# Performance work log

Hardware: AMD Instinct MI355X
Metric: run time of the kernel (lower is better)

## Reference

```python
import jax, jax.numpy as jnp
import numpy as np

N, E = 50000, 800000
D_IN, HID, HEADS, D_OUT = 128, 32, 4, 40
NEG_SLOPE = 0.2
BN_EPS = 1e-5


def gat_conv(x, src, dst, W, a_src, a_dst, b, heads, ch):
    """PyG-style GATConv (eval mode, self-loops already appended to src/dst)."""
    n = x.shape[0]
    h = (x @ W).reshape(n, heads, ch)                      # [N,H,C]
    al_src = jnp.einsum('nhc,hc->nh', h, a_src)            # [N,H]
    al_dst = jnp.einsum('nhc,hc->nh', h, a_dst)
    e = jax.nn.leaky_relu(al_src[src] + al_dst[dst], NEG_SLOPE)  # [Etot,H]
    # segment softmax over incoming edges of each dst node
    e_max = jax.ops.segment_max(e, dst, num_segments=n)
    e = jnp.exp(e - e_max[dst])
    denom = jax.ops.segment_sum(e, dst, num_segments=n)
    alpha = e / (denom[dst] + 1e-16)                        # [Etot,H]
    msg = h[src] * alpha[:, :, None]                        # [Etot,H,C]
    out = jax.ops.segment_sum(msg, dst, num_segments=n)     # [N,H,C]
    return out.reshape(n, heads * ch) + b


def bn_eval(x, g, b, m, v):
    return (x - m) * jax.lax.rsqrt(v + BN_EPS) * g + b


def setup_inputs() -> dict:
    key = jax.random.key(0)
    ks = jax.random.split(key, 24)
    p = lambda k, s: jax.random.normal(k, s, jnp.float32) * 0.1
    inp = {
        'x': jax.random.normal(ks[0], (N, D_IN), jnp.float32),
        'edge_index': jax.random.randint(ks[1], (2, E), 0, N),
        'W1': p(ks[2], (D_IN, HEADS * HID)),
        'a_src1': p(ks[3], (HEADS, HID)), 'a_dst1': p(ks[4], (HEADS, HID)),
        'b1': jnp.zeros((HEADS * HID,), jnp.float32),
        'W2': p(ks[5], (HEADS * HID, HEADS * HID)),
        'a_src2': p(ks[6], (HEADS, HID)), 'a_dst2': p(ks[7], (HEADS, HID)),
        'b2': jnp.zeros((HEADS * HID,), jnp.float32),
        'W3': p(ks[8], (HEADS * HID, D_OUT)),
        'a_src3': p(ks[9], (1, D_OUT)), 'a_dst3': p(ks[10], (1, D_OUT)),
        'b3': jnp.zeros((D_OUT,), jnp.float32),
        'bn1_g': jnp.ones((HEADS * HID,), jnp.float32),
        'bn1_b': jnp.zeros((HEADS * HID,), jnp.float32),
        'bn1_m': p(ks[11], (HEADS * HID,)),
        'bn1_v': jax.random.uniform(ks[12], (HEADS * HID,), jnp.float32) + 0.5,
        'bn2_g': jnp.ones((HEADS * HID,), jnp.float32),
        'bn2_b': jnp.zeros((HEADS * HID,), jnp.float32),
        'bn2_m': p(ks[13], (HEADS * HID,)),
        'bn2_v': jax.random.uniform(ks[14], (HEADS * HID,), jnp.float32) + 0.5,
    }
    return inp


def reference(x, edge_index, W1, a_src1, a_dst1, b1, W2, a_src2, a_dst2, b2,
              W3, a_src3, a_dst3, b3, bn1_g, bn1_b, bn1_m, bn1_v,
              bn2_g, bn2_b, bn2_m, bn2_v):
    n = x.shape[0]
    loop = jnp.arange(n, dtype=edge_index.dtype)
    src = jnp.concatenate([edge_index[0], loop])   # add self loops (PyG default)
    dst = jnp.concatenate([edge_index[1], loop])

    h = gat_conv(x, src, dst, W1, a_src1, a_dst1, b1, HEADS, HID)
    h = jax.nn.relu(h)
    h = bn_eval(h, bn1_g, bn1_b, bn1_m, bn1_v)      # dropout = identity (eval)

    h = gat_conv(h, src, dst, W2, a_src2, a_dst2, b2, HEADS, HID)
    h = jax.nn.relu(h)
    h = bn_eval(h, bn2_g, bn2_b, bn2_m, bn2_v)

    h = gat_conv(h, src, dst, W3, a_src3, a_dst3, b3, 1, D_OUT)
    return jax.nn.log_softmax(h, axis=1)
```

## Files before the change

### kernel.cpp

```cpp
#include <hip/hip_runtime.h>
#include <hip/hip_bf16.h>
#include <math.h>

using bf16 = __hip_bfloat16;
using frag8 = __attribute__((ext_vector_type(8))) short;
using f32x4 = __attribute__((ext_vector_type(4))) float;

#define LEAKY 0.2f
#define BN_EPS 1e-5f
#define NEGBIG -1e30f
#define BSHIFT 9

__device__ __forceinline__ float lrelu(float z){ return fmaxf(z, LEAKY * z); }
__device__ __forceinline__ float bflo(unsigned u){ return __uint_as_float(u << 16); }
__device__ __forceinline__ float bfhi(unsigned u){ return __uint_as_float(u & 0xffff0000u); }
__device__ __forceinline__ unsigned pk(float a, float b){
  unsigned ua = __float_as_uint(a), ub = __float_as_uint(b);
  ua += 0x7fffu + ((ua >> 16) & 1u);
  ub += 0x7fffu + ((ub >> 16) & 1u);
  return (ua >> 16) | (ub & 0xffff0000u);
}
__device__ __forceinline__ float ldf(const void* p, size_t i, int isbf){
  if (isbf) return (float)((const bf16*)p)[i];
  return ((const float*)p)[i];
}

union U4F8 { uint4 u; frag8 f; };

__device__ __forceinline__ frag8 load_a_pairs(const unsigned* __restrict__ X2, int node, int k0){
  U4F8 v; v.u = *((const uint4*)(X2 + (size_t)node*64 + (k0 >> 1))); return v.f;
}
__device__ __forceinline__ frag8 load_a_f32(const float* __restrict__ X, int node, int k0){
  float4 q0 = *((const float4*)(X + (size_t)node*128 + k0));
  float4 q1 = *((const float4*)(X + (size_t)node*128 + k0 + 4));
  U4F8 v; v.u = make_uint4(pk(q0.x,q0.y), pk(q0.z,q0.w), pk(q1.x,q1.y), pk(q1.z,q1.w));
  return v.f;
}

__global__ void init_detect(int* bcnt, const unsigned short* __restrict__ w1bits,
                            int* flag){
  __shared__ int cntr;
  if (threadIdx.x == 0) cntr = 0;
  bcnt[threadIdx.x] = 0;
  __syncthreads();
  unsigned u = w1bits[threadIdx.x * 2];
  int e = (u >> 7) & 0xff;
  atomicAdd(&cntr, (e >= 64 && e <= 140) ? 1 : 0);
  __syncthreads();
  if (threadIdx.x == 0) *flag = (cntr >= 160) ? 1 : 0;
}

__global__ __launch_bounds__(256) void wtrans(
    const void* __restrict__ W1, const void* __restrict__ W2,
    const void* __restrict__ W3, const int* __restrict__ flagp,
    unsigned short* __restrict__ WT1, unsigned short* __restrict__ WT2,
    unsigned short* __restrict__ WT3){
  const int isbf = *flagp;
  const int g = blockIdx.x*256 + threadIdx.x;
  if (g < 16384){
    int k = g >> 7, nn = g & 127;
    unsigned short v1, v2;
    if (isbf){
      v1 = ((const unsigned short*)W1)[g];
      v2 = ((const unsigned short*)W2)[g];
    } else {
      v1 = (unsigned short)(pk(((const float*)W1)[g], 0.f) & 0xffffu);
      v2 = (unsigned short)(pk(((const float*)W2)[g], 0.f) & 0xffffu);
    }
    WT1[nn*128 + k] = v1;
    WT2[nn*128 + k] = v2;
  }
  if (g < 8192){
    int c = g & 63, k = g >> 6;
    if (c < 48){
      unsigned short v = 0;
      if (c < 40){
        if (isbf) v = ((const unsigned short*)W3)[k*40 + c];
        else      v = (unsigned short)(pk(((const float*)W3)[k*40 + c], 0.f) & 0xffffu);
      }
      WT3[c*128 + k] = v;
    }
  }
}

__global__ __launch_bounds__(256) void hist(const int* __restrict__ dst,
                                            int* bcnt, int e, int n){
  __shared__ int lb[256];
  const int t = threadIdx.x;
  lb[t] = 0;
  __syncthreads();
  const int c0 = blockIdx.x*4096;
  const int lim = min(4096, e - c0);
  for (int i = t; i < lim; i += 256){
    int d = dst[c0 + i];
    if ((unsigned)d < (unsigned)n)
      atomicAdd(&lb[min(d >> BSHIFT, 255)], 1);
  }
  __syncthreads();
  if (lb[t]) atomicAdd(&bcnt[t], lb[t]);
}

__global__ void bscan(const int* __restrict__ bcnt, int* bstart, int* bpos){
  __shared__ int s[256];
  int t = threadIdx.x;
  int v = bcnt[t];
  s[t] = v;
  __syncthreads();
  for (int off = 1; off < 256; off <<= 1){
    int x = (t >= off) ? s[t-off] : 0;
    __syncthreads();
    s[t] += x;
    __syncthreads();
  }
  int st = s[t] - v;
  bstart[t] = st;
  bpos[t] = st;
}

__global__ __launch_bounds__(256) void bsort(const int* __restrict__ src,
                                             const int* __restrict__ dst,
                                             int* bpos, int2* __restrict__ ebuf,
                                             int e, int n){
  __shared__ int lh[256], lo[256], gb[256];
  __shared__ int tot_s;
  __shared__ int2 buf[4096];
  const int t = threadIdx.x;
  const int c0 = blockIdx.x*4096;
  if (c0 >= e) return;
  const int lim = min(4096, e - c0);
  lh[t] = 0;
  __syncthreads();
  int2 ev[16]; int bk[16];
  #pragma unroll
  for (int j = 0; j < 16; ++j){
    const int i = j*256 + t;
    const bool valid = i < lim;
    int s = 0, d = 0;
    if (valid){ s = src[c0 + i]; d = dst[c0 + i]; }
    ev[j] = make_int2(s, d);
    bk[j] = (valid && (unsigned)d < (unsigned)n) ? min(d >> BSHIFT, 255) : -1;
    if (bk[j] >= 0) atomicAdd(&lh[bk[j]], 1);
  }
  __syncthreads();
  const int v = lh[t];
  lo[t] = v;
  __syncthreads();
  for (int off = 1; off < 256; off <<= 1){
    int x = (t >= off) ? lo[t-off] : 0;
    __syncthreads();
    lo[t] += x;
    __syncthreads();
  }
  if (t == 255) tot_s = lo[255];
  lo[t] -= v;
  if (v) gb[t] = atomicAdd(&bpos[t], v);
  lh[t] = 0;
  __syncthreads();
  #pragma unroll
  for (int j = 0; j < 16; ++j){
    if (bk[j] >= 0){
      int r = atomicAdd(&lh[bk[j]], 1);
      buf[lo[bk[j]] + r] = ev[j];
    }
  }
  __syncthreads();
  const int tot = tot_s;
  for (int i = t; i < tot; i += 256){
    int2 sd = buf[i];
    int b = min(sd.y >> BSHIFT, 255);
    ebuf[gb[b] + (i - lo[b])] = sd;
  }
}

__global__ __launch_bounds__(256) void bfinal(const int2* __restrict__ ebuf,
    const int* __restrict__ bstart, const int* __restrict__ bpos,
    int* __restrict__ cnt, int* __restrict__ start, int* __restrict__ col, int n){
  __shared__ int deg[512], off[512], ps[256];
  const int b = blockIdx.x, t = threadIdx.x;
  const int n0 = b << BSHIFT;
  const int e0 = bstart[b], e1 = bpos[b];
  deg[t] = 0; deg[t + 256] = 0;
  __syncthreads();
  for (int i = e0 + t; i < e1; i += 256)
    atomicAdd(&deg[ebuf[i].y - n0], 1);
  __syncthreads();
  int p = deg[2*t] + deg[2*t + 1];
  ps[t] = p;
  __syncthreads();
  for (int o = 1; o < 256; o <<= 1){
    int x = (t >= o) ? ps[t - o] : 0;
    __syncthreads();
    ps[t] += x;
    __syncthreads();
  }
  int ex = ps[t] - p;
  off[2*t]     = ex;
  off[2*t + 1] = ex + deg[2*t];
  __syncthreads();
  #pragma unroll
  for (int j = t; j < 512; j += 256){
    int node = n0 + j;
    if (node < n){ cnt[node] = deg[j]; start[node] = e0 + off[j]; }
  }
  __syncthreads();
  for (int i = e0 + t; i < e1; i += 256){
    int2 sd = ebuf[i];
    int r = atomicAdd(&off[sd.y - n0], 1);
    col[e0 + r] = sd.x;
  }
}

__global__ __launch_bounds__(256) void gemm_al_mfma(
    const void* __restrict__ X, int xkind,
    const unsigned short* __restrict__ WT,
    const void* __restrict__ Wsrc, const void* __restrict__ Wdst,
    const int* __restrict__ flagp,
    unsigned* __restrict__ H2, float* __restrict__ AL, float* __restrict__ AD,
    int n, int ntiles)
{
  const int isbf = *flagp;
  const int t = threadIdx.x;
  const int w = t >> 6;
  const int lane = t & 63;
  const int m = lane & 15, quad = lane >> 4;

  frag8 bf[4][2];
  #pragma unroll
  for (int s = 0; s < 4; ++s)
    #pragma unroll
    for (int ct = 0; ct < 2; ++ct){
      int colc = w*32 + ct*16 + m;
      int k0 = s*32 + quad*8;
      U4F8 v; v.u = *((const uint4*)(WT + colc*128 + k0));
      bf[s][ct] = v.f;
    }
  float avv[2], dvv[2];
  #pragma unroll
  for (int ct = 0; ct < 2; ++ct){
    int colc = w*32 + ct*16 + m;
    avv[ct] = ldf(Wsrc, colc, isbf);
    dvv[ct] = ldf(Wdst, colc, isbf);
  }
  const bool pairs = (xkind == 1) || isbf;

  for (int tile = blockIdx.x; tile < ntiles; tile += gridDim.x){
    const int mb = tile*16;
    int nodeA = mb + m; if (nodeA >= n) nodeA = n - 1;
    frag8 af[4];
    #pragma unroll
    for (int s = 0; s < 4; ++s){
      int k0 = s*32 + quad*8;
      af[s] = pairs ? load_a_pairs((const unsigned*)X, nodeA, k0)
                    : load_a_f32((const float*)X, nodeA, k0);
    }
    f32x4 acc0 = {0.f,0.f,0.f,0.f}, acc1 = {0.f,0.f,0.f,0.f};
    #pragma unroll
    for (int s = 0; s < 4; ++s){
      acc0 = __builtin_amdgcn_mfma_f32_16x16x32_bf16(af[s], bf[s][0], acc0, 0,0,0);
      acc1 = __builtin_amdgcn_mfma_f32_16x16x32_bf16(af[s], bf[s][1], acc1, 0,0,0);
    }
    #pragma unroll
    for (int r = 0; r < 4; ++r){
      int g = mb + quad*4 + r;
      float v0 = acc0[r], v1 = acc1[r];
      unsigned u0 = pk(v0, __shfl_xor(v0, 1));
      unsigned u1 = pk(v1, __shfl_xor(v1, 1));
      bool ok = g < n;
      if (((lane & 1) == 0) && ok){
        H2[(size_t)g*64 + w*16 + (m >> 1)]     = u0;
        H2[(size_t)g*64 + w*16 + 8 + (m >> 1)] = u1;
      }
      float s1 = v0*avv[0] + v1*avv[1];
      float s2 = v0*dvv[0] + v1*dvv[1];
      s1 += __shfl_xor(s1,1); s1 += __shfl_xor(s1,2); s1 += __shfl_xor(s1,4); s1 += __shfl_xor(s1,8);
      s2 += __shfl_xor(s2,1); s2 += __shfl_xor(s2,2); s2 += __shfl_xor(s2,4); s2 += __shfl_xor(s2,8);
      if (m == 0 && ok){ AL[g*4 + w] = s1; AD[g*4 + w] = s2; }
    }
  }
}

__global__ __launch_bounds__(256) void gemm3_mfma(
    const unsigned* __restrict__ X2, const unsigned short* __restrict__ WT,
    const void* __restrict__ Wsrc, const void* __restrict__ Wdst,
    const int* __restrict__ flagp,
    unsigned* __restrict__ H3, float* __restrict__ AL, float* __restrict__ AD,
    int n, int ntiles)
{
  const int isbf = *flagp;
  const int t = threadIdx.x;
  const int w = t >> 6;
  const int lane = t & 63;
  const int m = lane & 15, quad = lane >> 4;

  frag8 bf[4][3];
  float avv[3], dvv[3];
  #pragma unroll
  for (int ct = 0; ct < 3; ++ct){
    int colc = ct*16 + m;
    #pragma unroll
    for (int s = 0; s < 4; ++s){
      int k0 = s*32 + quad*8;
      U4F8 v; v.u = *((const uint4*)(WT + colc*128 + k0));
      bf[s][ct] = v.f;
    }
    avv[ct] = (colc < 40) ? ldf(Wsrc, colc, isbf) : 0.f;
    dvv[ct] = (colc < 40) ? ldf(Wdst, colc, isbf) : 0.f;
  }

  for (int tg = blockIdx.x; tg*4 < ntiles; tg += gridDim.x){
    const int tile = tg*4 + w;
    if (tile >= ntiles) continue;
    const int mb = tile*16;
    int nodeA = mb + m; if (nodeA >= n) nodeA = n - 1;
    frag8 af[4];
    #pragma unroll
    for (int s = 0; s < 4; ++s)
      af[s] = load_a_pairs(X2, nodeA, s*32 + quad*8);
    f32x4 acc[3];
    #pragma unroll
    for (int ct = 0; ct < 3; ++ct) acc[ct] = (f32x4){0.f,0.f,0.f,0.f};
    #pragma unroll
    for (int s = 0; s < 4; ++s){
      acc[0] = __builtin_amdgcn_mfma_f32_16x16x32_bf16(af[s], bf[s][0], acc[0], 0,0,0);
      acc[1] = __builtin_amdgcn_mfma_f32_16x16x32_bf16(af[s], bf[s][1], acc[1], 0,0,0);
      acc[2] = __builtin_amdgcn_mfma_f32_16x16x32_bf16(af[s], bf[s][2], acc[2], 0,0,0);
    }
    #pragma unroll
    for (int r = 0; r < 4; ++r){
      int g = mb + quad*4 + r;
      bool ok = g < n;
      float ps = 0.f, pd = 0.f;
      #pragma unroll
      for (int ct = 0; ct < 3; ++ct){
        float v = acc[ct][r];
        ps += v*avv[ct]; pd += v*dvv[ct];
        unsigned u = pk(v, __shfl_xor(v, 1));
        bool stok = ((lane & 1) == 0) && ok && (ct < 2 || m < 8);
        if (stok) H3[(size_t)g*20 + ct*8 + (m >> 1)] = u;
      }
      ps += __shfl_xor(ps,1); ps += __shfl_xor(ps,2); ps += __shfl_xor(ps,4); ps += __shfl_xor(ps,8);
      pd += __shfl_xor(pd,1); pd += __shfl_xor(pd,2); pd += __shfl_xor(pd,4); pd += __shfl_xor(pd,8);
      if (m == 0 && ok){ AL[g] = ps; AD[g] = pd; }
    }
  }
}

__global__ __launch_bounds__(256) void agg4(
    const unsigned* __restrict__ H2,
    const float* __restrict__ ALf, const float* __restrict__ ADf,
    const int* __restrict__ cnt, const int* __restrict__ start, const int* __restrict__ col,
    const void* __restrict__ bias, const void* __restrict__ bng, const void* __restrict__ bnb,
    const void* __restrict__ bnm,  const void* __restrict__ bnv,
    const int* __restrict__ flagp,
    unsigned* __restrict__ Hout, int n)
{
  const int isbf = *flagp;
  const int wave = threadIdx.x >> 6;
  const int lane = threadIdx.x & 63;
  const int node = blockIdx.x*4 + wave;
  if (node >= n) return;
  const int head = lane >> 4;
  const float ad = ADf[node*4 + head];
  const int eu = (lane >> 2) & 7;
  const int eh = lane & 3;
  const float ade = ADf[node*4 + eh];
  const int base = start[node], deg = cnt[node];

  float accL, accH, l;
  {
    float e = __expf(lrelu(ALf[node*4 + head] + ad));
    unsigned h = H2[(size_t)node*64 + lane];
    l = e; accL = e * bflo(h); accH = e * bfhi(h);
  }

  const int nb8 = deg >> 3, rem = deg & 7;
  int sva[8], svb[8];
  if (nb8){
    #pragma unroll
    for (int u = 0; u < 8; ++u) sva[u] = col[base + u];
  } else if (rem){
    const int lim = rem - 1;
    #pragma unroll
    for (int u = 0; u < 8; ++u) sva[u] = col[base + (u < lim ? u : lim)];
  }
  for (int b = 0; b < nb8; ++b){
    unsigned hv[8];
    #pragma unroll
    for (int u = 0; u < 8; ++u) hv[u] = H2[(size_t)sva[u]*64 + lane];
    float ave = ALf[sva[eu]*4 + eh];
    if (b + 1 < nb8){
      const int nbb = base + (b + 1)*8;
      #pragma unroll
      for (int u = 0; u < 8; ++u) svb[u] = col[nbb + u];
    } else if (rem){
      const int tb = base + nb8*8, lim = rem - 1;
      #pragma unroll
      for (int u = 0; u < 8; ++u) svb[u] = col[tb + (u < lim ? u : lim)];
    }
    float ew = __expf(lrelu(ave + ade));
    #pragma unroll
    for (int u = 0; u < 8; ++u){
      float e = __shfl(ew, (u << 2) + head);
      l += e;
      accL = fmaf(e, bflo(hv[u]), accL);
      accH = fmaf(e, bfhi(hv[u]), accH);
    }
    #pragma unroll
    for (int u = 0; u < 8; ++u) sva[u] = svb[u];
  }
  if (rem){
    unsigned hv[8];
    #pragma unroll
    for (int u = 0; u < 8; ++u) hv[u] = H2[(size_t)sva[u]*64 + lane];
    float ave = ALf[sva[eu]*4 + eh];
    float ew = __expf(lrelu(ave + ade));
    #pragma unroll
    for (int u = 0; u < 8; ++u){
      float e = (u < rem) ? __shfl(ew, (u << 2) + head) : 0.f;
      l += e;
      accL = fmaf(e, bflo(hv[u]), accL);
      accH = fmaf(e, bfhi(hv[u]), accH);
    }
  }

  const float rl = 1.f / l;
  const int c0 = 2*lane, c1 = c0 + 1;
  float v0 = fmaxf(accL*rl + ldf(bias,c0,isbf), 0.f);
  v0 = (v0 - ldf(bnm,c0,isbf)) * rsqrtf(ldf(bnv,c0,isbf) + BN_EPS) * ldf(bng,c0,isbf) + ldf(bnb,c0,isbf);
  float v1 = fmaxf(accH*rl + ldf(bias,c1,isbf), 0.f);
  v1 = (v1 - ldf(bnm,c1,isbf)) * rsqrtf(ldf(bnv,c1,isbf) + BN_EPS) * ldf(bng,c1,isbf) + ldf(bnb,c1,isbf);
  Hout[(size_t)node*64 + lane] = pk(v0, v1);
}

__global__ __launch_bounds__(256) void agg1(
    const unsigned* __restrict__ H3,
    const float* __restrict__ AL, const float* __restrict__ AD,
    const int* __restrict__ cnt, const int* __restrict__ start, const int* __restrict__ col,
    const void* __restrict__ b3, const int* __restrict__ flagp,
    void* __restrict__ out, int n)
{
  const int isbf = *flagp;
  const int t = threadIdx.x;
  const int p = t & 31;
  const int node = blockIdx.x*8 + (t >> 5);
  if (node >= n) return;
  const float ad = AD[node];
  const bool act = p < 20;
  const int eu = p & 7;
  const int base = start[node], deg = cnt[node];

  float accL, accH, l;
  {
    float e = __expf(lrelu(AL[node] + ad));
    unsigned h = act ? H3[(size_t)node*20 + p] : 0u;
    l = e; accL = e * bflo(h); accH = e * bfhi(h);
  }

  const int nb8 = deg >> 3, rem = deg & 7;
  int sva[8], svb[8];
  if (nb8){
    #pragma unroll
    for (int u = 0; u < 8; ++u) sva[u] = col[base + u];
  } else if (rem){
    const int lim = rem - 1;
    #pragma unroll
    for (int u = 0; u < 8; ++u) sva[u] = col[base + (u < lim ? u : lim)];
  }
  for (int b = 0; b < nb8; ++b){
    unsigned hv[8];
    #pragma unroll
    for (int u = 0; u < 8; ++u) hv[u] = act ? H3[(size_t)sva[u]*20 + p] : 0u;
    float ave = AL[sva[eu]];
    if (b + 1 < nb8){
      const int nbb = base + (b + 1)*8;
      #pragma unroll
      for (int u = 0; u < 8; ++u) svb[u] = col[nbb + u];
    } else if (rem){
      const int tb = base + nb8*8, lim = rem - 1;
      #pragma unroll
      for (int u = 0; u < 8; ++u) svb[u] = col[tb + (u < lim ? u : lim)];
    }
    float ew = __expf(lrelu(ave + ad));
    #pragma unroll
    for (int u = 0; u < 8; ++u){
      float e = __shfl(ew, u, 32);
      l += e;
      accL = fmaf(e, bflo(hv[u]), accL);
      accH = fmaf(e, bfhi(hv[u]), accH);
    }
    #pragma unroll
    for (int u = 0; u < 8; ++u) sva[u] = svb[u];
  }
  if (rem){
    unsigned hv[8];
    #pragma unroll
    for (int u = 0; u < 8; ++u) hv[u] = act ? H3[(size_t)sva[u]*20 + p] : 0u;
    float ave = AL[sva[eu]];
    float ew = __expf(lrelu(ave + ad));
    #pragma unroll
    for (int u = 0; u < 8; ++u){
      float e = (u < rem) ? __shfl(ew, u, 32) : 0.f;
      l += e;
      accL = fmaf(e, bflo(hv[u]), accL);
      accH = fmaf(e, bfhi(hv[u]), accH);
    }
  }

  const float rl = 1.f / l;
  const int c0 = 2*p;
  float z0 = act ? (accL*rl + ldf(b3, c0,     isbf)) : NEGBIG;
  float z1 = act ? (accH*rl + ldf(b3, c0 + 1, isbf)) : NEGBIG;
  float mx = fmaxf(z0, z1);
  #pragma unroll
  for (int off = 1; off < 32; off <<= 1) mx = fmaxf(mx, __shfl_xor(mx, off));
  float pp = act ? (__expf(z0 - mx) + __expf(z1 - mx)) : 0.f;
  float sum = pp;
  #pragma unroll
  for (int off = 1; off < 32; off <<= 1) sum += __shfl_xor(sum, off);
  if (act){
    float lg = __logf(sum);
    float r0 = z0 - mx - lg, r1 = z1 - mx - lg;
    if (isbf) ((unsigned*)out)[(size_t)node*20 + p] = pk(r0, r1);
    else      ((float2*)out)[(size_t)node*20 + p] = make_float2(r0, r1);
  }
}

extern "C" void kernel_launch(void* const* d_in, const int* in_sizes, int n_in,
                              void* d_out, int out_size, void* d_ws, size_t ws_size,
                              hipStream_t stream)
{
  (void)n_in; (void)out_size; (void)ws_size;
  const void* x    = d_in[0];
  const int*  ei   = (const int*)d_in[1];
  const void* W1   = d_in[2];
  const void* as1  = d_in[3];
  const void* ad1  = d_in[4];
  const void* b1   = d_in[5];
  const void* W2   = d_in[6];
  const void* as2  = d_in[7];
  const void* ad2  = d_in[8];
  const void* b2   = d_in[9];
  const void* W3   = d_in[10];
  const void* as3  = d_in[11];
  const void* ad3  = d_in[12];
  const void* b3   = d_in[13];
  const void* bn1g = d_in[14];
  const void* bn1b = d_in[15];
  const void* bn1m = d_in[16];
  const void* bn1v = d_in[17];
  const void* bn2g = d_in[18];
  const void* bn2b = d_in[19];
  const void* bn2m = d_in[20];
  const void* bn2v = d_in[21];

  const int N  = in_sizes[0] / 128;
  const int E  = in_sizes[1] / 2;
  const int ntiles = (N + 15) / 16;

  char* w = (char*)d_ws;
  size_t off = 0;
  auto alloc = [&](size_t bytes)->char*{
    char* p = w + off; off = (off + bytes + 255) & ~(size_t)255; return p;
  };
  unsigned* H2A = (unsigned*)alloc((size_t)N*64*4);
  unsigned* H2B = (unsigned*)alloc((size_t)N*64*4);
  unsigned* H3p = (unsigned*)alloc((size_t)N*20*4);
  float* AL   = (float*)alloc((size_t)N*4*4);
  float* AD   = (float*)alloc((size_t)N*4*4);
  int*   cnt   = (int*)alloc((size_t)N*4);
  int*   start = (int*)alloc((size_t)N*4);
  int*   col   = (int*)alloc((size_t)E*4);
  int2*  ebuf  = (int2*)alloc((size_t)E*8);
  unsigned short* WT1 = (unsigned short*)alloc(16384*2);
  unsigned short* WT2 = (unsigned short*)alloc(16384*2);
  unsigned short* WT3 = (unsigned short*)alloc(48*128*2);
  int*   bcnt  = (int*)alloc(1024);
  int*   bstart= (int*)alloc(1024);
  int*   bpos  = (int*)alloc(1024);
  int*   flag  = (int*)alloc(256);

  const int* srcp = ei;
  const int* dstp = ei + E;

  const int nbCH = (E + 4095)/4096;
  const int NB = (N + 511) >> BSHIFT;
  const int bb = (N + 3)/4;
  const int bb1 = (N + 7)/8;
  int g1 = ntiles < 625 ? ntiles : 625;
  int g3 = (ntiles + 3)/4; if (g3 > 400) g3 = 400;

  init_detect<<<1,256,0,stream>>>(bcnt, (const unsigned short*)W1, flag);
  wtrans<<<64,256,0,stream>>>(W1, W2, W3, flag, WT1, WT2, WT3);
  hist<<<nbCH,256,0,stream>>>(dstp, bcnt, E, N);
  bscan<<<1,256,0,stream>>>(bcnt, bstart, bpos);
  bsort<<<nbCH,256,0,stream>>>(srcp, dstp, bpos, ebuf, E, N);
  bfinal<<<NB,256,0,stream>>>(ebuf, bstart, bpos, cnt, start, col, N);

  gemm_al_mfma<<<g1,256,0,stream>>>(x, 0, WT1, as1, ad1, flag, H2A, AL, AD, N, ntiles);
  agg4<<<bb,256,0,stream>>>(H2A, AL, AD, cnt, start, col,
                            b1, bn1g, bn1b, bn1m, bn1v, flag, H2B, N);
  gemm_al_mfma<<<bb ? g1 : g1,256,0,stream>>>(H2B, 1, WT2, as2, ad2, flag, H2A, AL, AD, N, ntiles);
  agg4<<<bb,256,0,stream>>>(H2A, AL, AD, cnt, start, col,
                            b2, bn2g, bn2b, bn2m, bn2v, flag, H2B, N);
  gemm3_mfma<<<g3,256,0,stream>>>((const unsigned*)H2B, WT3, as3, ad3, flag, H3p, AL, AD, N, ntiles);
  agg1<<<bb1,256,0,stream>>>(H3p, AL, AD, cnt, start, col, b3, flag, d_out, N);
}
```

Before: 322.6 us.

## Scatter bucketed edges directly, scalarize CSR loads, enlarge GEMM grids

The bucket-sort kernel drops its shared-memory staging buffer and local prefix scan. Each edge is now written straight to global memory at its bucket offset plus a shared atomic rank. This cuts shared-memory use and barriers but makes the global writes less coalesced. Separately, the per-node start and degree values in agg4 are forced into scalar registers with readfirstlane, and the GEMM grid caps are raised so every tile gets its own block.

```diff
diff --git a/kernel.cpp b/kernel.cpp
--- a/kernel.cpp
+++ b/kernel.cpp
@@ -117,13 +117,11 @@
   bpos[t] = st;
 }
 
-__global__ __launch_bounds__(256) void bsort(const int* __restrict__ src,
-                                             const int* __restrict__ dst,
-                                             int* bpos, int2* __restrict__ ebuf,
-                                             int e, int n){
-  __shared__ int lh[256], lo[256], gb[256];
-  __shared__ int tot_s;
-  __shared__ int2 buf[4096];
+__global__ __launch_bounds__(256) void bres(const int* __restrict__ src,
+                                            const int* __restrict__ dst,
+                                            int* bpos, int2* __restrict__ ebuf,
+                                            int e, int n){
+  __shared__ int lh[256], gb[256];
   const int t = threadIdx.x;
   const int c0 = blockIdx.x*4096;
   if (c0 >= e) return;
@@ -143,32 +141,16 @@
   }
   __syncthreads();
   const int v = lh[t];
-  lo[t] = v;
-  __syncthreads();
-  for (int off = 1; off < 256; off <<= 1){
-    int x = (t >= off) ? lo[t-off] : 0;
-    __syncthreads();
-    lo[t] += x;
-    __syncthreads();
-  }
-  if (t == 255) tot_s = lo[255];
-  lo[t] -= v;
   if (v) gb[t] = atomicAdd(&bpos[t], v);
+  __syncthreads();
   lh[t] = 0;
   __syncthreads();
   #pragma unroll
   for (int j = 0; j < 16; ++j){
     if (bk[j] >= 0){
       int r = atomicAdd(&lh[bk[j]], 1);
-      buf[lo[bk[j]] + r] = ev[j];
-    }
-  }
-  __syncthreads();
-  const int tot = tot_s;
-  for (int i = t; i < tot; i += 256){
-    int2 sd = buf[i];
-    int b = min(sd.y >> BSHIFT, 255);
-    ebuf[gb[b] + (i - lo[b])] = sd;
+      ebuf[gb[bk[j]] + r] = ev[j];
+    }
   }
 }
 
@@ -364,7 +346,8 @@
   const int eu = (lane >> 2) & 7;
   const int eh = lane & 3;
   const float ade = ADf[node*4 + eh];
-  const int base = start[node], deg = cnt[node];
+  const int base = __builtin_amdgcn_readfirstlane(start[node]);
+  const int deg  = __builtin_amdgcn_readfirstlane(cnt[node]);
 
   float accL, accH, l;
   {
@@ -586,20 +569,20 @@
   const int NB = (N + 511) >> BSHIFT;
   const int bb = (N + 3)/4;
   const int bb1 = (N + 7)/8;
-  int g1 = ntiles < 625 ? ntiles : 625;
-  int g3 = (ntiles + 3)/4; if (g3 > 400) g3 = 400;
+  int g1 = ntiles;
+  int g3 = (ntiles + 3)/4; if (g3 > 800) g3 = 800;
 
   init_detect<<<1,256,0,stream>>>(bcnt, (const unsigned short*)W1, flag);
   wtrans<<<64,256,0,stream>>>(W1, W2, W3, flag, WT1, WT2, WT3);
   hist<<<nbCH,256,0,stream>>>(dstp, bcnt, E, N);
   bscan<<<1,256,0,stream>>>(bcnt, bstart, bpos);
-  bsort<<<nbCH,256,0,stream>>>(srcp, dstp, bpos, ebuf, E, N);
+  bres<<<nbCH,256,0,stream>>>(srcp, dstp, bpos, ebuf, E, N);
   bfinal<<<NB,256,0,stream>>>(ebuf, bstart, bpos, cnt, start, col, N);
 
   gemm_al_mfma<<<g1,256,0,stream>>>(x, 0, WT1, as1, ad1, flag, H2A, AL, AD, N, ntiles);
   agg4<<<bb,256,0,stream>>>(H2A, AL, AD, cnt, start, col,
                             b1, bn1g, bn1b, bn1m, bn1v, flag, H2B, N);
-  gemm_al_mfma<<<bb ? g1 : g1,256,0,stream>>>(H2B, 1, WT2, as2, ad2, flag, H2A, AL, AD, N, ntiles);
+  gemm_al_mfma<<<g1,256,0,stream>>>(H2B, 1, WT2, as2, ad2, flag, H2A, AL, AD, N, ntiles);
   agg4<<<bb,256,0,stream>>>(H2A, AL, AD, cnt, start, col,
                             b2, bn2g, bn2b, bn2m, bn2v, flag, H2B, N);
   gemm3_mfma<<<g3,256,0,stream>>>((const unsigned*)H2B, WT3, as3, ad3, flag, H3p, AL, AD, N, ntiles);
```

After: 320.6 us. No clear change (-0.6%).
